# Kernel tuning notes

Measured on AMD Instinct MI355X. Metric: run time of the kernel, lower is better.

Reference implementation:

```python
import jax, jax.numpy as jnp
import numpy as np

B, T, N, M, D = 4, 64, 32, 32, 128  # batch, time, price points, liquidity points, feature dim


def setup_inputs() -> dict:
    key = jax.random.key(0)
    ks = jax.random.split(key, 6)
    w = lambda k, shape: jax.random.normal(k, shape, jnp.float32) * 0.05
    return {
        "price": jax.random.normal(ks[0], (B, T, N, D), jnp.float32),
        "liquid": jax.random.normal(ks[1], (B, T, M, D), jnp.float32),
        "W_p": w(ks[2], (D, D)), "b_p": jnp.zeros((D,), jnp.float32),
        "W_v": w(ks[3], (D, D)), "b_v": jnp.zeros((D,), jnp.float32),
        "W1": w(ks[4], (4 * D, D)), "b1": jnp.zeros((D,), jnp.float32),
        "W2": w(ks[5], (D, D)), "b2": jnp.zeros((D,), jnp.float32),
    }


def reference(price, liquid, W_p, b_p, W_v, b_v, W1, b1, W2, b2):
    # proj_p / proj_v
    p = price @ W_p + b_p    # [B, T, N, D]
    v = liquid @ W_v + b_v   # [B, T, M, D]
    p4 = p[:, :, :, None, :]  # [B, T, N, 1, D]
    v4 = v[:, :, None, :, :]  # [B, T, 1, M, D]
    prod = p4 * v4            # [B, T, N, M, D]
    absdiff = jnp.abs(p4 - v4)
    full = (p.shape[0], p.shape[1], p.shape[2], v.shape[2], p.shape[3])
    pair = jnp.concatenate(
        [jnp.broadcast_to(p4, full), jnp.broadcast_to(v4, full), prod, absdiff],
        axis=-1,
    )  # [B, T, N, M, 4D]
    h = jax.nn.silu(pair @ W1 + b1)  # [B, T, N, M, D]
    grid = h @ W2 + b2               # [B, T, N, M, D]
    return grid.reshape(grid.shape[0], grid.shape[1], grid.shape[2] * grid.shape[3], grid.shape[4])
```

## Files before the change

kernel.cpp:

```cpp
#include <hip/hip_runtime.h>


typedef short  short8  __attribute__((ext_vector_type(8)));
typedef float  f32x4   __attribute__((ext_vector_type(4)));
typedef float  f32x16  __attribute__((ext_vector_type(16)));

#define DEV static __device__ __forceinline__

DEV float bf2f(unsigned short h) {
  unsigned u = ((unsigned)h) << 16;
  float f;
  __builtin_memcpy(&f, &u, 4);
  return f;
}
DEV unsigned short f2bf(float f) {
  unsigned u;
  __builtin_memcpy(&u, &f, 4);
  unsigned r = (u + 0x7FFFu + ((u >> 16) & 1u)) >> 16;
  return (unsigned short)r;
}
DEV unsigned pk2(float fh, float fl) {
  return __builtin_amdgcn_perm(__float_as_uint(fh), __float_as_uint(fl), 0x07060302u);
}
DEV float lo16(unsigned u) { return __uint_as_float(u << 16); }
DEV float hi16(unsigned u) { return __uint_as_float(u & 0xFFFF0000u); }

union V8 { uint4 u; unsigned a[4]; short8 s; };

__global__ void k0_prep(const float* __restrict__ Wp, const float* __restrict__ bp,
                        const float* __restrict__ Wv, const float* __restrict__ bv,
                        const float* __restrict__ W1, const float* __restrict__ b1,
                        const float* __restrict__ W2,
                        unsigned short* __restrict__ w1cd, unsigned short* __restrict__ w2sw,
                        unsigned short* __restrict__ wpsw, unsigned short* __restrict__ gpsw,
                        unsigned short* __restrict__ wvsw, unsigned short* __restrict__ gvsw,
                        float* __restrict__ c1) {
  int t = blockIdx.x * 256 + threadIdx.x;
  if (t < 32768) {
    int j = t & 7, lane = (t >> 3) & 63, r2 = t >> 9;
    int ct = r2 & 3, kt = r2 >> 2;
    int k = kt * 16 + (lane >> 5) * 8 + j;
    int c = ct * 32 + (lane & 31);
    w1cd[t] = f2bf(W1[(256 + k) * 128 + c]);
  } else if (t < 114688) {
    int e = t - 32768;
    int sec = e >> 14;
    int f = e & 16383;
    int j = f & 7, lane = (f >> 3) & 63, r2 = f >> 9;
    if (sec == 0) {
      int ct = r2 & 3, kt = r2 >> 2;
      int k = kt * 16 + (lane >> 5) * 8 + j;
      int c = ct * 32 + (lane & 31);
      w2sw[f] = f2bf(W2[k * 128 + c]);
    } else {
      int kt = r2 & 3, ct = r2 >> 2;
      int k = kt * 32 + ((lane >> 4) & 3) * 8 + j;
      int n = ct * 16 + (lane & 15);
      if (sec == 1) {
        wpsw[f] = f2bf(Wp[k * 128 + n]);
      } else if (sec == 2) {
        float s = 0.f;
        for (int e2 = 0; e2 < 128; e2++) s += Wp[k * 128 + e2] * W1[e2 * 128 + n];
        gpsw[f] = f2bf(s);
      } else if (sec == 3) {
        wvsw[f] = f2bf(Wv[k * 128 + n]);
      } else {
        float s = 0.f;
        for (int e2 = 0; e2 < 128; e2++) s += Wv[k * 128 + e2] * W1[(128 + e2) * 128 + n];
        gvsw[f] = f2bf(s);
      }
    }
  } else if (t < 114816) {
    int c = t - 114688;
    float s = b1[c];
    for (int e2 = 0; e2 < 128; e2++)
      s += bp[e2] * W1[e2 * 128 + c] + bv[e2] * W1[(128 + e2) * 128 + c];
    c1[c] = s;
  }
}

__global__ __launch_bounds__(256, 2) void k1_proj(
    const float* __restrict__ price, const float* __restrict__ liquid,
    const float* __restrict__ bp, const float* __restrict__ bv, const float* __restrict__ c1,
    const unsigned short* __restrict__ wpsw, const unsigned short* __restrict__ gpsw,
    const unsigned short* __restrict__ wvsw, const unsigned short* __restrict__ gvsw,
    unsigned short* __restrict__ pbf, unsigned short* __restrict__ vbf,
    float* __restrict__ pAc, unsigned short* __restrict__ vbsw) {
  __shared__ __align__(16) unsigned short sA[128 * 136];
  int b = blockIdx.x;
  int chunk = b >> 2, sel = b & 3;
  int side = sel >> 1, half = sel & 1;
  int rowbase = chunk * 128;
  const float* src = side ? liquid : price;
  const unsigned short* bsw = side ? (half ? gvsw : wvsw) : (half ? gpsw : wpsw);
  int tid = threadIdx.x;

#pragma unroll
  for (int i = 0; i < 16; i++) {
    int e4 = i * 256 + tid;
    int row = e4 >> 5, c4 = (e4 & 31) * 4;
    float4 f = *(const float4*)(src + (rowbase + row) * 128 + c4);
    uint2 pk;
    pk.x = pk2(f.y, f.x);
    pk.y = pk2(f.w, f.z);
    *(uint2*)&sA[row * 136 + c4] = pk;
  }
  __syncthreads();

  int lane = tid & 63, w = tid >> 6;
  int l15 = lane & 15, q4 = lane >> 4;
  f32x4 acc[2][8] = {};
#pragma unroll
  for (int kt = 0; kt < 4; kt++) {
    short8 a0 = *(const short8*)&sA[(w * 32 + l15) * 136 + kt * 32 + q4 * 8];
    short8 a1 = *(const short8*)&sA[(w * 32 + 16 + l15) * 136 + kt * 32 + q4 * 8];
#pragma unroll
    for (int ct = 0; ct < 8; ct++) {
      short8 bfr = *(const short8*)(bsw + ((ct * 4 + kt) * 64 + lane) * 8);
      acc[0][ct] = __builtin_amdgcn_mfma_f32_16x16x32_bf16(a0, bfr, acc[0][ct], 0, 0, 0);
      acc[1][ct] = __builtin_amdgcn_mfma_f32_16x16x32_bf16(a1, bfr, acc[1][ct], 0, 0, 0);
    }
  }

#pragma unroll
  for (int rg = 0; rg < 2; rg++) {
#pragma unroll
    for (int ct = 0; ct < 8; ct++) {
      int col = ct * 16 + l15;
      int lrow0 = w * 32 + rg * 16 + q4 * 4;
#pragma unroll
      for (int ri = 0; ri < 4; ri++) {
        int grow = rowbase + lrow0 + ri;
        float val = acc[rg][ct][ri];
        if (side == 0) {
          if (half == 0) pbf[grow * 128 + col] = f2bf(val + bp[col]);
          else           pAc[grow * 128 + col] = val + c1[col];
        } else {
          if (half == 0) vbf[grow * 128 + col] = f2bf(val + bv[col]);
          else {
            int btl = grow >> 5, m = grow & 31;
            int idx = btl * 4096 +
                      ((((m >> 4) * 4 + (col >> 5)) * 64) + ((m >> 3) & 1) * 32 + (col & 31)) * 8 +
                      (m & 7);
            vbsw[idx] = f2bf(val);
          }
        }
      }
    }
  }
}

__global__ __launch_bounds__(256, 2) void k2_fused(
    const unsigned short* __restrict__ pbf, const unsigned short* __restrict__ vbf,
    const float* __restrict__ pAc, const unsigned short* __restrict__ w1cd,
    const unsigned short* __restrict__ vbsw, const unsigned short* __restrict__ w2sw,
    const float* __restrict__ b2, float* __restrict__ out) {
  __shared__ __align__(16) unsigned short sVf[4096];
  __shared__ __align__(16) unsigned short sP[8 * 136];
  __shared__ __align__(16) unsigned short sHt[4][32 * 72];
  int bt = blockIdx.x >> 2, n0 = (blockIdx.x & 3) * 8;
  int tid = threadIdx.x;

  if (tid < 128) {
    int row = tid >> 4, seg = tid & 15;
    *(uint4*)&sP[row * 136 + seg * 8] = *(const uint4*)(pbf + (bt * 32 + n0 + row) * 128 + seg * 8);
  }
#pragma unroll
  for (int g2 = 0; g2 < 2; g2++) {
    int g = tid * 2 + g2;
    int m = g & 31, k0 = (g >> 5) * 8;
    *(uint4*)&sVf[g * 8] = *(const uint4*)(vbf + (bt * 32 + m) * 128 + k0);
  }
  __syncthreads();

  int lane = tid & 63, w = tid >> 6;
  int m31 = lane & 31, hi = lane >> 5;
  int na = 2 * w, nb = 2 * w + 1;
  const unsigned short* vbswt = vbsw + bt * 4096;

  float pa0[4], pa1[4], bia[4];
#pragma unroll
  for (int ct = 0; ct < 4; ct++) {
    pa0[ct] = pAc[(bt * 32 + n0 + na) * 128 + ct * 32 + m31];
    pa1[ct] = pAc[(bt * 32 + n0 + nb) * 128 + ct * 32 + m31];
    bia[ct] = b2[ct * 32 + m31];
  }

  f32x16 acc0[4] = {};
  f32x16 acc1[4] = {};

#pragma unroll
  for (int kt = 0; kt < 8; kt++) {
    V8 vf, p0, p1, x0, y0, x1, y1;
    vf.u = *(const uint4*)&sVf[((kt * 2 + hi) * 32 + m31) * 8];
    p0.u = *(const uint4*)&sP[na * 136 + kt * 16 + hi * 8];
    p1.u = *(const uint4*)&sP[nb * 136 + kt * 16 + hi * 8];
#pragma unroll
    for (int i = 0; i < 4; i++) {
      float vl = lo16(vf.a[i]), vh = hi16(vf.a[i]);
      float al = lo16(p0.a[i]), ah = hi16(p0.a[i]);
      float cl = lo16(p1.a[i]), ch = hi16(p1.a[i]);
      x0.a[i] = pk2(ah * vh, al * vl);
      y0.a[i] = pk2(fabsf(ah - vh), fabsf(al - vl));
      x1.a[i] = pk2(ch * vh, cl * vl);
      y1.a[i] = pk2(fabsf(ch - vh), fabsf(cl - vl));
    }
    const unsigned short* bxb = w1cd + (kt * 4) * 512;
    const unsigned short* byb = w1cd + ((kt + 8) * 4) * 512;
#pragma unroll
    for (int ct = 0; ct < 4; ct++) {
      short8 bx = *(const short8*)(bxb + ct * 512 + lane * 8);
      short8 by = *(const short8*)(byb + ct * 512 + lane * 8);
      acc0[ct] = __builtin_amdgcn_mfma_f32_32x32x16_bf16(x0.s, bx, acc0[ct], 0, 0, 0);
      acc1[ct] = __builtin_amdgcn_mfma_f32_32x32x16_bf16(x1.s, bx, acc1[ct], 0, 0, 0);
      acc0[ct] = __builtin_amdgcn_mfma_f32_32x32x16_bf16(y0.s, by, acc0[ct], 0, 0, 0);
      acc1[ct] = __builtin_amdgcn_mfma_f32_32x32x16_bf16(y1.s, by, acc1[ct], 0, 0, 0);
    }
  }

#pragma unroll
  for (int kt2 = 0; kt2 < 2; kt2++) {
    short8 indf;
#pragma unroll
    for (int j = 0; j < 8; j++)
      indf[j] = (short)(((kt2 * 16 + hi * 8 + j) == m31) ? 0x3F80 : 0);
#pragma unroll
    for (int ct = 0; ct < 4; ct++) {
      short8 bi = *(const short8*)(vbswt + (kt2 * 4 + ct) * 512 + lane * 8);
      acc0[ct] = __builtin_amdgcn_mfma_f32_32x32x16_bf16(indf, bi, acc0[ct], 0, 0, 0);
      acc1[ct] = __builtin_amdgcn_mfma_f32_32x32x16_bf16(indf, bi, acc1[ct], 0, 0, 0);
    }
  }

#pragma unroll
  for (int ct = 0; ct < 4; ct++) {
#pragma unroll
    for (int i = 0; i < 16; i++) { acc0[ct][i] += pa0[ct]; acc1[ct][i] += pa1[ct]; }
  }

  unsigned short* sh = &sHt[w][0];
  auto tail = [&](const f32x16* A, int n) {
    f32x16 o[4] = {};
#pragma unroll
    for (int p = 0; p < 2; p++) {
#pragma unroll
      for (int c2 = 0; c2 < 2; c2++) {
        int ct = p * 2 + c2;
#pragma unroll
        for (int reg = 0; reg < 16; reg++) {
          float z = A[ct][reg];
          float hv = z * __builtin_amdgcn_rcpf(1.f + __expf(-z));
          int mr = (reg & 3) + 8 * (reg >> 2) + 4 * hi;
          sh[mr * 72 + c2 * 32 + m31] = (unsigned short)(__float_as_uint(hv) >> 16);
        }
      }
#pragma unroll
      for (int kt = 0; kt < 4; kt++) {
        int ktg = p * 4 + kt;
        short8 hf = *(const short8*)&sh[m31 * 72 + kt * 16 + hi * 8];
#pragma unroll
        for (int ct = 0; ct < 4; ct++) {
          short8 wf = *(const short8*)(w2sw + ((ktg * 4 + ct) * 64 + lane) * 8);
          o[ct] = __builtin_amdgcn_mfma_f32_32x32x16_bf16(hf, wf, o[ct], 0, 0, 0);
        }
      }
    }
    int rowb = bt * 1024 + n * 32;
#pragma unroll
    for (int ct = 0; ct < 4; ct++) {
#pragma unroll
      for (int reg = 0; reg < 16; reg++) {
        int mr = (reg & 3) + 8 * (reg >> 2) + 4 * hi;
        out[(rowb + mr) * 128 + ct * 32 + m31] = o[ct][reg] + bia[ct];
      }
    }
  };
  tail(acc0, n0 + na);
  tail(acc1, n0 + nb);
}

extern "C" void kernel_launch(void* const* d_in, const int* in_sizes, int n_in,
                              void* d_out, int out_size, void* d_ws, size_t ws_size,
                              hipStream_t stream) {
  const float* price  = (const float*)d_in[0];
  const float* liquid = (const float*)d_in[1];
  const float* Wp     = (const float*)d_in[2];
  const float* bp     = (const float*)d_in[3];
  const float* Wv     = (const float*)d_in[4];
  const float* bv     = (const float*)d_in[5];
  const float* W1     = (const float*)d_in[6];
  const float* b1     = (const float*)d_in[7];
  const float* W2     = (const float*)d_in[8];
  const float* b2     = (const float*)d_in[9];

  char* ws = (char*)d_ws;
  unsigned short* w1cd = (unsigned short*)(ws + 0);
  unsigned short* w2sw = (unsigned short*)(ws + 65536);
  unsigned short* wpsw = (unsigned short*)(ws + 98304);
  unsigned short* gpsw = (unsigned short*)(ws + 131072);
  unsigned short* wvsw = (unsigned short*)(ws + 163840);
  unsigned short* gvsw = (unsigned short*)(ws + 196608);
  float*          c1   = (float*)(ws + 229376);
  unsigned short* pbf  = (unsigned short*)(ws + 262144);
  unsigned short* vbf  = (unsigned short*)(ws + 2359296);
  float*          pAc  = (float*)(ws + 4456448);
  unsigned short* vbsw = (unsigned short*)(ws + 8650752);

  hipLaunchKernelGGL(k0_prep, dim3(449), dim3(256), 0, stream,
                     Wp, bp, Wv, bv, W1, b1, W2, w1cd, w2sw, wpsw, gpsw, wvsw, gvsw, c1);
  hipLaunchKernelGGL(k1_proj, dim3(256), dim3(256), 0, stream,
                     price, liquid, bp, bv, c1, wpsw, gpsw, wvsw, gvsw, pbf, vbf, pAc, vbsw);
  hipLaunchKernelGGL(k2_fused, dim3(1024), dim3(256), 0, stream,
                     pbf, vbf, pAc, w1cd, vbsw, w2sw, b2, (float*)d_out);
}
```

Measured before the change: 242.7 us.

## Halve per-wave work in fused pair kernel to raise occupancy

Each wave now processes one price row instead of two, so the fused kernel launches twice as many blocks, each covering 4 price rows instead of 8. Accumulator register use is halved, and launch bounds are raised to allow 3 blocks per CU for better latency hiding. The cost is that each block reloads the full liquidity tile into shared memory, and the weight fragment loads are amortized over half as many MFMAs.

After: 213.0 us. -12.2%, faster.

```diff
diff --git a/kernel.cpp b/kernel.cpp
--- a/kernel.cpp
+++ b/kernel.cpp
@@ -150,20 +150,20 @@
   }
 }
 
-__global__ __launch_bounds__(256, 2) void k2_fused(
+__global__ __launch_bounds__(256, 3) void k2_fused(
     const unsigned short* __restrict__ pbf, const unsigned short* __restrict__ vbf,
     const float* __restrict__ pAc, const unsigned short* __restrict__ w1cd,
     const unsigned short* __restrict__ vbsw, const unsigned short* __restrict__ w2sw,
     const float* __restrict__ b2, float* __restrict__ out) {
   __shared__ __align__(16) unsigned short sVf[4096];
-  __shared__ __align__(16) unsigned short sP[8 * 136];
+  __shared__ __align__(16) unsigned short sP[4 * 136];
   __shared__ __align__(16) unsigned short sHt[4][32 * 72];
-  int bt = blockIdx.x >> 2, n0 = (blockIdx.x & 3) * 8;
+  int bt = blockIdx.x >> 3, slab = (blockIdx.x & 7) * 4;
   int tid = threadIdx.x;
 
-  if (tid < 128) {
+  if (tid < 64) {
     int row = tid >> 4, seg = tid & 15;
-    *(uint4*)&sP[row * 136 + seg * 8] = *(const uint4*)(pbf + (bt * 32 + n0 + row) * 128 + seg * 8);
+    *(uint4*)&sP[row * 136 + seg * 8] = *(const uint4*)(pbf + (bt * 32 + slab + row) * 128 + seg * 8);
   }
 #pragma unroll
   for (int g2 = 0; g2 < 2; g2++) {
@@ -175,35 +175,29 @@
 
   int lane = tid & 63, w = tid >> 6;
   int m31 = lane & 31, hi = lane >> 5;
-  int na = 2 * w, nb = 2 * w + 1;
+  int n = slab + w;
   const unsigned short* vbswt = vbsw + bt * 4096;
 
-  float pa0[4], pa1[4], bia[4];
+  float pa[4], bia[4];
 #pragma unroll
   for (int ct = 0; ct < 4; ct++) {
-    pa0[ct] = pAc[(bt * 32 + n0 + na) * 128 + ct * 32 + m31];
-    pa1[ct] = pAc[(bt * 32 + n0 + nb) * 128 + ct * 32 + m31];
+    pa[ct]  = pAc[(bt * 32 + n) * 128 + ct * 32 + m31];
     bia[ct] = b2[ct * 32 + m31];
   }
 
-  f32x16 acc0[4] = {};
-  f32x16 acc1[4] = {};
+  f32x16 acc[4] = {};
 
 #pragma unroll
   for (int kt = 0; kt < 8; kt++) {
-    V8 vf, p0, p1, x0, y0, x1, y1;
+    V8 vf, pp, x, y;
     vf.u = *(const uint4*)&sVf[((kt * 2 + hi) * 32 + m31) * 8];
-    p0.u = *(const uint4*)&sP[na * 136 + kt * 16 + hi * 8];
-    p1.u = *(const uint4*)&sP[nb * 136 + kt * 16 + hi * 8];
+    pp.u = *(const uint4*)&sP[w * 136 + kt * 16 + hi * 8];
 #pragma unroll
     for (int i = 0; i < 4; i++) {
       float vl = lo16(vf.a[i]), vh = hi16(vf.a[i]);
-      float al = lo16(p0.a[i]), ah = hi16(p0.a[i]);
-      float cl = lo16(p1.a[i]), ch = hi16(p1.a[i]);
-      x0.a[i] = pk2(ah * vh, al * vl);
-      y0.a[i] = pk2(fabsf(ah - vh), fabsf(al - vl));
-      x1.a[i] = pk2(ch * vh, cl * vl);
-      y1.a[i] = pk2(fabsf(ch - vh), fabsf(cl - vl));
+      float al = lo16(pp.a[i]), ah = hi16(pp.a[i]);
+      x.a[i] = pk2(ah * vh, al * vl);
+      y.a[i] = pk2(fabsf(ah - vh), fabsf(al - vl));
     }
     const unsigned short* bxb = w1cd + (kt * 4) * 512;
     const unsigned short* byb = w1cd + ((kt + 8) * 4) * 512;
@@ -211,10 +205,8 @@
     for (int ct = 0; ct < 4; ct++) {
       short8 bx = *(const short8*)(bxb + ct * 512 + lane * 8);
       short8 by = *(const short8*)(byb + ct * 512 + lane * 8);
-      acc0[ct] = __builtin_amdgcn_mfma_f32_32x32x16_bf16(x0.s, bx, acc0[ct], 0, 0, 0);
-      acc1[ct] = __builtin_amdgcn_mfma_f32_32x32x16_bf16(x1.s, bx, acc1[ct], 0, 0, 0);
-      acc0[ct] = __builtin_amdgcn_mfma_f32_32x32x16_bf16(y0.s, by, acc0[ct], 0, 0, 0);
-      acc1[ct] = __builtin_amdgcn_mfma_f32_32x32x16_bf16(y1.s, by, acc1[ct], 0, 0, 0);
+      acc[ct] = __builtin_amdgcn_mfma_f32_32x32x16_bf16(x.s, bx, acc[ct], 0, 0, 0);
+      acc[ct] = __builtin_amdgcn_mfma_f32_32x32x16_bf16(y.s, by, acc[ct], 0, 0, 0);
     }
   }
 
@@ -227,56 +219,46 @@
 #pragma unroll
     for (int ct = 0; ct < 4; ct++) {
       short8 bi = *(const short8*)(vbswt + (kt2 * 4 + ct) * 512 + lane * 8);
-      acc0[ct] = __builtin_amdgcn_mfma_f32_32x32x16_bf16(indf, bi, acc0[ct], 0, 0, 0);
-      acc1[ct] = __builtin_amdgcn_mfma_f32_32x32x16_bf16(indf, bi, acc1[ct], 0, 0, 0);
-    }
-  }
-
-#pragma unroll
-  for (int ct = 0; ct < 4; ct++) {
-#pragma unroll
-    for (int i = 0; i < 16; i++) { acc0[ct][i] += pa0[ct]; acc1[ct][i] += pa1[ct]; }
+      acc[ct] = __builtin_amdgcn_mfma_f32_32x32x16_bf16(indf, bi, acc[ct], 0, 0, 0);
+    }
   }
 
   unsigned short* sh = &sHt[w][0];
-  auto tail = [&](const f32x16* A, int n) {
-    f32x16 o[4] = {};
-#pragma unroll
-    for (int p = 0; p < 2; p++) {
-#pragma unroll
-      for (int c2 = 0; c2 < 2; c2++) {
-        int ct = p * 2 + c2;
-#pragma unroll
-        for (int reg = 0; reg < 16; reg++) {
-          float z = A[ct][reg];
-          float hv = z * __builtin_amdgcn_rcpf(1.f + __expf(-z));
-          int mr = (reg & 3) + 8 * (reg >> 2) + 4 * hi;
-          sh[mr * 72 + c2 * 32 + m31] = (unsigned short)(__float_as_uint(hv) >> 16);
-        }
-      }
-#pragma unroll
-      for (int kt = 0; kt < 4; kt++) {
-        int ktg = p * 4 + kt;
-        short8 hf = *(const short8*)&sh[m31 * 72 + kt * 16 + hi * 8];
-#pragma unroll
-        for (int ct = 0; ct < 4; ct++) {
-          short8 wf = *(const short8*)(w2sw + ((ktg * 4 + ct) * 64 + lane) * 8);
-          o[ct] = __builtin_amdgcn_mfma_f32_32x32x16_bf16(hf, wf, o[ct], 0, 0, 0);
-        }
-      }
-    }
-    int rowb = bt * 1024 + n * 32;
-#pragma unroll
-    for (int ct = 0; ct < 4; ct++) {
+  f32x16 o[4] = {};
+#pragma unroll
+  for (int p = 0; p < 2; p++) {
+#pragma unroll
+    for (int c2 = 0; c2 < 2; c2++) {
+      int ct = p * 2 + c2;
 #pragma unroll
       for (int reg = 0; reg < 16; reg++) {
+        float z = acc[ct][reg] + pa[ct];
+        float hv = z * __builtin_amdgcn_rcpf(1.f + __expf(-z));
         int mr = (reg & 3) + 8 * (reg >> 2) + 4 * hi;
-        out[(rowb + mr) * 128 + ct * 32 + m31] = o[ct][reg] + bia[ct];
-      }
-    }
-  };
-  tail(acc0, n0 + na);
-  tail(acc1, n0 + nb);
+        sh[mr * 72 + c2 * 32 + m31] = (unsigned short)(__float_as_uint(hv) >> 16);
+      }
+    }
+#pragma unroll
+    for (int kt = 0; kt < 4; kt++) {
+      int ktg = p * 4 + kt;
+      short8 hf = *(const short8*)&sh[m31 * 72 + kt * 16 + hi * 8];
+#pragma unroll
+      for (int ct2 = 0; ct2 < 4; ct2++) {
+        short8 wf = *(const short8*)(w2sw + ((ktg * 4 + ct2) * 64 + lane) * 8);
+        o[ct2] = __builtin_amdgcn_mfma_f32_32x32x16_bf16(hf, wf, o[ct2], 0, 0, 0);
+      }
+    }
+  }
+
+  int rowb = bt * 1024 + n * 32;
+#pragma unroll
+  for (int ct2 = 0; ct2 < 4; ct2++) {
+#pragma unroll
+    for (int reg = 0; reg < 16; reg++) {
+      int mr = (reg & 3) + 8 * (reg >> 2) + 4 * hi;
+      out[(rowb + mr) * 128 + ct2 * 32 + m31] = o[ct2][reg] + bia[ct2];
+    }
+  }
 }
 
 extern "C" void kernel_launch(void* const* d_in, const int* in_sizes, int n_in,
@@ -310,6 +292,6 @@
                      Wp, bp, Wv, bv, W1, b1, W2, w1cd, w2sw, wpsw, gpsw, wvsw, gvsw, c1);
   hipLaunchKernelGGL(k1_proj, dim3(256), dim3(256), 0, stream,
                      price, liquid, bp, bv, c1, wpsw, gpsw, wvsw, gvsw, pbf, vbf, pAc, vbsw);
-  hipLaunchKernelGGL(k2_fused, dim3(1024), dim3(256), 0, stream,
+  hipLaunchKernelGGL(k2_fused, dim3(2048), dim3(256), 0, stream,
                      pbf, vbf, pAc, w1cd, vbsw, w2sw, b2, (float*)d_out);
 }
```
